# Kernel optimization log

Measured on AMD Instinct MI355X. Metric: run time of the kernel, lower is better.

## Reference

```python
import jax, jax.numpy as jnp
import numpy as np

N, DIN = 8192, 768
DH1, DO1 = 64, 64
DH2, DO2 = 32, 64


def setup_inputs() -> dict:
    key = jax.random.key(0)
    ks = jax.random.split(key, 12)
    s = lambda *sh: 0.02
    inp = {
        "X": jax.random.normal(ks[0], (N, DIN), jnp.float32),
        "A": jax.random.randint(ks[1], (N, N), 0, 2, jnp.int32),
        # GAT layer 1: W (din->dh), a (2dh), W2 (dh->dout) + bias
        "W1": jax.random.normal(ks[2], (DIN, DH1), jnp.float32) * 0.02,
        "a1": jax.random.normal(ks[3], (2 * DH1,), jnp.float32) * 0.02,
        "W21": jax.random.normal(ks[4], (DH1, DO1), jnp.float32) * 0.02,
        "b21": jnp.zeros((DO1,), jnp.float32),
        # GAT layer 2
        "Wg2": jax.random.normal(ks[5], (DO1, DH2), jnp.float32) * 0.02,
        "a2": jax.random.normal(ks[6], (2 * DH2,), jnp.float32) * 0.02,
        "W22": jax.random.normal(ks[7], (DH2, DO2), jnp.float32) * 0.02,
        "b22": jnp.zeros((DO2,), jnp.float32),
        # MLP head: 64 -> 64 -> 2
        "M1": jax.random.normal(ks[8], (DO2, 64), jnp.float32) * 0.02,
        "bm1": jnp.zeros((64,), jnp.float32),
        "M2": jax.random.normal(ks[9], (64, 2), jnp.float32) * 0.02,
        "bm2": jnp.zeros((2,), jnp.float32),
    }
    return inp


def _tiny_gat(X, A, W, a, W2, b2):
    # H = X @ W; e_ij = a . [H_i, H_j] = H_i@a_src + H_j@a_dst (same math,
    # no N x N x 2dh intermediate)
    H = X @ W                      # [N, dh]
    dh = W.shape[1]
    e = (H @ a[:dh])[:, None] + (H @ a[dh:])[None, :]   # [N, N]
    e = jnp.where(A == 0, jnp.float32(-1e9), e)
    alpha = jax.nn.softmax(e, axis=1)                   # softmax over neighbors j
    Z = alpha @ H                                       # [N, dh]
    return jax.nn.elu(Z @ W2 + b2)


def reference(X, A, W1, a1, W21, b21, Wg2, a2, W22, b22, M1, bm1, M2, bm2):
    Z = _tiny_gat(X, A, W1, a1, W21, b21)    # [N, 64]
    Z = _tiny_gat(Z, A, Wg2, a2, W22, b22)   # [N, 64]
    g = Z.mean(axis=0)                       # [64]
    h = jax.nn.relu(g @ M1 + bm1)
    return h @ M2 + bm2                      # [2]
```

## Files before the change

### kernel.cpp

```cpp
#include <hip/hip_runtime.h>


#define NN 8192

typedef __attribute__((ext_vector_type(8))) short s16x8;
typedef __attribute__((ext_vector_type(4))) float f32x4;
union V16 { uint4 u; s16x8 s; };

static constexpr size_t OFF_WBITS = 0;
static constexpr size_t OFF_GT1H  = (size_t)8 << 20;
static constexpr size_t OFF_GT1L  = ((size_t)9 << 20) + 512 * 1024;
static constexpr size_t OFF_GT2H  = (size_t)11 << 20;
static constexpr size_t OFF_GT2L  = (size_t)12 << 20;
static constexpr size_t OFF_GPART = (size_t)13 << 20;
static constexpr size_t OFF_NUMP  = (size_t)16 << 20;
static constexpr size_t OFF_DP    = (size_t)40 << 20;

__device__ __forceinline__ float elu_f(float x) {
    return x > 0.f ? x : expm1f(x);
}
__device__ __forceinline__ unsigned int bf16_rne(float x) {
    unsigned int u = __float_as_uint(x);
    return (u + 0x7FFFu + ((u >> 16) & 1u)) >> 16;
}
__device__ __forceinline__ unsigned int split_pack(float g) {
    unsigned int hi = bf16_rne(g);
    float fhi = __uint_as_float(hi << 16);
    unsigned int lo = bf16_rne(g - fhi);
    return (hi << 16) | lo;
}
__device__ __forceinline__ void split3(float f, unsigned int& h, unsigned int& m,
                                       unsigned int& l) {
    h = bf16_rne(f);
    float fh = __uint_as_float(h << 16);
    float r1 = f - fh;
    m = bf16_rne(r1);
    float fm = __uint_as_float(m << 16);
    l = bf16_rne(r1 - fm);
}
__device__ __forceinline__ unsigned int bits2bf(unsigned int b2) {
    return (b2 & 1u) * 0x3F80u + (b2 & 2u) * 0x1FC00000u;
}

__global__ __launch_bounds__(256) void k_xw1m(const float* __restrict__ X,
                                              const float* __restrict__ W1,
                                              float* __restrict__ Dp) {
    __shared__ unsigned int fh[6144];
    __shared__ unsigned int fl[6144];
    const int tid = threadIdx.x, wv = tid >> 6, lane = tid & 63;
    const int ks = blockIdx.y;
    for (int i = tid; i < 6144; i += 256) {
        const int feat = i & 63, kp = i >> 6;
        const int kg = ks * 192 + 2 * kp;
        float w0 = W1[(size_t)kg * 64 + feat];
        float w1 = W1[(size_t)(kg + 1) * 64 + feat];
        unsigned int h0 = bf16_rne(w0);
        unsigned int l0 = bf16_rne(w0 - __uint_as_float(h0 << 16));
        unsigned int h1 = bf16_rne(w1);
        unsigned int l1 = bf16_rne(w1 - __uint_as_float(h1 << 16));
        const int mt = feat >> 4, n = feat & 15;
        const int ktl = kp >> 4, rem = kp & 15, quad = rem >> 2, q = rem & 3;
        const int idx = ((mt * 6 + ktl) * 64 + quad * 16 + n) * 4 + q;
        fh[idx] = h0 | (h1 << 16);
        fl[idx] = l0 | (l1 << 16);
    }
    __syncthreads();
    const int n = lane & 15, quad = lane >> 4;
    const int node = blockIdx.x * 64 + wv * 16 + n;
    const int ntg = blockIdx.x * 4 + wv;
    f32x4 acc[4];
#pragma unroll
    for (int mt = 0; mt < 4; ++mt) acc[mt] = (f32x4){0.f, 0.f, 0.f, 0.f};
    const float4* X4 = (const float4*)X;
    for (int kk = 0; kk < 6; ++kk) {
        const int ktg = ks * 6 + kk;
        float4 x01 = X4[(size_t)node * 192 + ktg * 8 + quad * 2];
        float4 x23 = X4[(size_t)node * 192 + ktg * 8 + quad * 2 + 1];
        float xf[8] = {x01.x, x01.y, x01.z, x01.w, x23.x, x23.y, x23.z, x23.w};
        V16 bh, bm, bl;
        unsigned int* bhp = (unsigned int*)&bh.u;
        unsigned int* bmp = (unsigned int*)&bm.u;
        unsigned int* blp = (unsigned int*)&bl.u;
#pragma unroll
        for (int q = 0; q < 4; ++q) {
            unsigned int h0, m0, l0, h1, m1, l1;
            split3(xf[2 * q], h0, m0, l0);
            split3(xf[2 * q + 1], h1, m1, l1);
            bhp[q] = h0 | (h1 << 16);
            bmp[q] = m0 | (m1 << 16);
            blp[q] = l0 | (l1 << 16);
        }
#pragma unroll
        for (int mt = 0; mt < 4; ++mt) {
            const int base = ((mt * 6 + kk) * 64 + lane) * 4;
            V16 awh, awl;
            awh.u = *(const uint4*)&fh[base];
            awl.u = *(const uint4*)&fl[base];
            acc[mt] = __builtin_amdgcn_mfma_f32_16x16x32_bf16(awh.s, bh.s, acc[mt], 0, 0, 0);
            acc[mt] = __builtin_amdgcn_mfma_f32_16x16x32_bf16(awh.s, bm.s, acc[mt], 0, 0, 0);
            acc[mt] = __builtin_amdgcn_mfma_f32_16x16x32_bf16(awh.s, bl.s, acc[mt], 0, 0, 0);
            acc[mt] = __builtin_amdgcn_mfma_f32_16x16x32_bf16(awl.s, bh.s, acc[mt], 0, 0, 0);
            acc[mt] = __builtin_amdgcn_mfma_f32_16x16x32_bf16(awl.s, bm.s, acc[mt], 0, 0, 0);
        }
    }
#pragma unroll
    for (int mt = 0; mt < 4; ++mt)
        *(f32x4*)&Dp[(size_t)(((ks * 4 + mt) * 512 + ntg) * 64 + lane) * 4] = acc[mt];
}

__global__ __launch_bounds__(256) void k_xcomb(const float* __restrict__ Dp,
                                               const float* __restrict__ a1,
                                               unsigned int* __restrict__ Gt1h,
                                               unsigned int* __restrict__ Gt1l) {
    __shared__ float Hsh[64][33];
    __shared__ float us[32];
    const int tid = threadIdx.x;
    if (tid < 128) {
        const int ntl = tid >> 6, lane = tid & 63;
        const int n = lane & 15, quad = lane >> 4;
        const int ntg = blockIdx.x * 2 + ntl;
        float dpart = 0.f;
#pragma unroll
        for (int mt = 0; mt < 4; ++mt) {
            float v[4] = {0.f, 0.f, 0.f, 0.f};
#pragma unroll
            for (int ksp = 0; ksp < 4; ++ksp) {
                const float* p = &Dp[(size_t)(((ksp * 4 + mt) * 512 + ntg) * 64 + lane) * 4];
                v[0] += p[0]; v[1] += p[1]; v[2] += p[2]; v[3] += p[3];
            }
#pragma unroll
            for (int r = 0; r < 4; ++r) {
                int feat = mt * 16 + quad * 4 + r;
                Hsh[feat][ntl * 16 + n] = v[r];
                dpart += v[r] * a1[64 + feat];
            }
        }
        dpart += __shfl_xor(dpart, 16);
        dpart += __shfl_xor(dpart, 32);
        float uu = expf(dpart);
        if (lane < 16) us[ntl * 16 + lane] = uu;
    }
    __syncthreads();
    {
        const int mt = tid >> 6, lane = tid & 63;
        const int feat = mt * 16 + (lane & 15), quad = lane >> 4;
        uint4 hv, lv;
        unsigned int g0, g1;
#define PACK_Q(Q, FX)                                                   \
        {                                                               \
            int j0 = quad * 8 + 2 * Q;                                  \
            g0 = split_pack(us[j0] * Hsh[feat][j0]);                    \
            g1 = split_pack(us[j0 + 1] * Hsh[feat][j0 + 1]);            \
            hv.FX = (g0 >> 16) | (g1 & 0xFFFF0000u);                    \
            lv.FX = (g0 & 0xFFFFu) | (g1 << 16);                        \
        }
        PACK_Q(0, x) PACK_Q(1, y) PACK_Q(2, z) PACK_Q(3, w)
#undef PACK_Q
        size_t base = ((size_t)(mt * 256 + blockIdx.x) * 64 + lane) * 4;
        *(uint4*)(Gt1h + base) = hv;
        *(uint4*)(Gt1l + base) = lv;
    }
    if (tid < 64) {
        const int ml = tid & 15, quad = tid >> 4;
        uint4 hv, lv;
        unsigned int g0, g1;
#define PACK_Q(Q, FX)                                                   \
        {                                                               \
            int j0 = quad * 8 + 2 * Q;                                  \
            if (ml == 0) { g0 = split_pack(us[j0]);                     \
                           g1 = split_pack(us[j0 + 1]); }               \
            else { g0 = 0; g1 = 0; }                                    \
            hv.FX = (g0 >> 16) | (g1 & 0xFFFF0000u);                    \
            lv.FX = (g0 & 0xFFFFu) | (g1 << 16);                        \
        }
        PACK_Q(0, x) PACK_Q(1, y) PACK_Q(2, z) PACK_Q(3, w)
#undef PACK_Q
        size_t base = ((size_t)(4 * 256 + blockIdx.x) * 64 + tid) * 4;
        *(uint4*)(Gt1h + base) = hv;
        *(uint4*)(Gt1l + base) = lv;
    }
}

__global__ __launch_bounds__(320) void k_attn1f(const int* __restrict__ A,
                                                const unsigned int* __restrict__ Gt1h,
                                                const unsigned int* __restrict__ Gt1l,
                                                unsigned int* __restrict__ Wb32,
                                                float* __restrict__ num1p) {
    __shared__ unsigned int bw[64 * 33];
    const int tid = threadIdx.x, wv = tid >> 6, lane = tid & 63;
    const int node0 = blockIdx.x * 64;
    const int kc = blockIdx.y;
    if (wv < 4) {
        unsigned short* msh = (unsigned short*)bw;
        for (int rr = 0; rr < 16; ++rr) {
            const int r = wv * 16 + rr;
            const int4* A4 = (const int4*)(A + (size_t)(node0 + r) * NN + kc * 1024 + lane * 16);
            int4 a0 = A4[0], a1 = A4[1], a2 = A4[2], a3 = A4[3];
            unsigned int m0 = 0;
            m0 |= ((a0.x != 0) << 0)  | ((a0.y != 0) << 1)  |
                  ((a0.z != 0) << 2)  | ((a0.w != 0) << 3);
            m0 |= ((a1.x != 0) << 4)  | ((a1.y != 0) << 5)  |
                  ((a1.z != 0) << 6)  | ((a1.w != 0) << 7);
            m0 |= ((a2.x != 0) << 8)  | ((a2.y != 0) << 9)  |
                  ((a2.z != 0) << 10) | ((a2.w != 0) << 11);
            m0 |= ((a3.x != 0) << 12) | ((a3.y != 0) << 13) |
                  ((a3.z != 0) << 14) | ((a3.w != 0) << 15);
            msh[r * 66 + lane] = (unsigned short)m0;
        }
    }
    __syncthreads();
    if (tid < 256) {
        const int r = tid >> 2, part = tid & 3;
        uint4 v0, v1;
        v0.x = bw[r * 33 + part * 8 + 0]; v0.y = bw[r * 33 + part * 8 + 1];
        v0.z = bw[r * 33 + part * 8 + 2]; v0.w = bw[r * 33 + part * 8 + 3];
        v1.x = bw[r * 33 + part * 8 + 4]; v1.y = bw[r * 33 + part * 8 + 5];
        v1.z = bw[r * 33 + part * 8 + 6]; v1.w = bw[r * 33 + part * 8 + 7];
        uint4* dst = (uint4*)(Wb32 + (size_t)(node0 + r) * 256 + kc * 32 + part * 8);
        dst[0] = v0; dst[1] = v1;
    }
    const int n = lane & 15, quad = lane >> 4;
    const int mt = wv;
    const int kt0 = kc * 32;
    f32x4 acc[4];
#pragma unroll
    for (int nt = 0; nt < 4; ++nt) acc[nt] = (f32x4){0.f, 0.f, 0.f, 0.f};
#pragma unroll 4
    for (int ks = 0; ks < 32; ++ks) {
        size_t base = ((size_t)(mt * 256 + kt0 + ks) * 64 + lane) * 4;
        V16 ah, al;
        ah.u = *(const uint4*)(Gt1h + base);
        al.u = *(const uint4*)(Gt1l + base);
#pragma unroll
        for (int nt = 0; nt < 4; ++nt) {
            unsigned int by8 = (bw[(nt * 16 + n) * 33 + ks] >> (quad * 8)) & 0xFFu;
            V16 bf;
            bf.u = make_uint4(bits2bf(by8), bits2bf(by8 >> 2),
                              bits2bf(by8 >> 4), bits2bf(by8 >> 6));
            acc[nt] = __builtin_amdgcn_mfma_f32_16x16x32_bf16(ah.s, bf.s, acc[nt], 0, 0, 0);
            acc[nt] = __builtin_amdgcn_mfma_f32_16x16x32_bf16(al.s, bf.s, acc[nt], 0, 0, 0);
        }
    }
    const int s = blockIdx.y;
#pragma unroll
    for (int nt = 0; nt < 4; ++nt) {
        const int node = node0 + nt * 16 + n;
        *(f32x4*)&num1p[((size_t)s * NN + node) * 80 + mt * 16 + quad * 4] = acc[nt];
    }
}

__global__ __launch_bounds__(256) void k_ep1(const float* __restrict__ num1p,
                                             const float* __restrict__ W21,
                                             const float* __restrict__ b21,
                                             const float* __restrict__ Wg2,
                                             const float* __restrict__ a2,
                                             unsigned int* __restrict__ Gt2h,
                                             unsigned int* __restrict__ Gt2l) {
    __shared__ float w21sh[64 * 64];
    __shared__ float wg2sh[64 * 32];
    __shared__ float zsh[4][64];
    __shared__ float osh[4][64];
    __shared__ unsigned int g2sh[32][9];
    __shared__ unsigned int u2sh[8];
    const int tid = threadIdx.x, wv = tid >> 6, lane = tid & 63;
    const int node0 = blockIdx.x * 8;
    {
        const float4* s4 = (const float4*)W21;
        float4* d4 = (float4*)w21sh;
        d4[tid] = s4[tid];
        d4[tid + 256] = s4[tid + 256];
        d4[tid + 512] = s4[tid + 512];
        d4[tid + 768] = s4[tid + 768];
        ((float4*)wg2sh)[tid] = ((const float4*)Wg2)[tid];
        ((float4*)wg2sh)[tid + 256] = ((const float4*)Wg2)[tid + 256];
    }
    const float bb = b21[lane];
    const int l32 = lane & 31;
    const float a2v = (lane < 32) ? a2[32 + l32] : 0.f;
    __syncthreads();
    for (int it = 0; it < 2; ++it) {
        const int node = node0 + wv * 2 + it;
        float sacc = 0.f, dnum = 0.f;
#pragma unroll
        for (int sp = 0; sp < 8; ++sp) {
            const float* base = &num1p[((size_t)sp * NN + node) * 80];
            sacc += base[lane];
            dnum += base[64];
        }
        zsh[wv][lane] = sacc / dnum;
        __builtin_amdgcn_wave_barrier();
        const float4* zv = (const float4*)&zsh[wv][0];
        float o0 = 0.f, o1 = 0.f;
#pragma unroll 4
        for (int c4 = 0; c4 < 16; ++c4) {
            float4 z4 = zv[c4];
            const int c = c4 * 4;
            o0 += z4.x * w21sh[(c + 0) * 64 + lane] + z4.y * w21sh[(c + 1) * 64 + lane];
            o1 += z4.z * w21sh[(c + 2) * 64 + lane] + z4.w * w21sh[(c + 3) * 64 + lane];
        }
        float o = elu_f(bb + o0 + o1);
        osh[wv][lane] = o;
        __builtin_amdgcn_wave_barrier();
        const float4* ov = (const float4*)&osh[wv][0];
        float h0 = 0.f, h1 = 0.f;
#pragma unroll 4
        for (int c4 = 0; c4 < 16; ++c4) {
            float4 o4 = ov[c4];
            const int c = c4 * 4;
            h0 += o4.x * wg2sh[(c + 0) * 32 + l32] + o4.y * wg2sh[(c + 1) * 32 + l32];
            h1 += o4.z * wg2sh[(c + 2) * 32 + l32] + o4.w * wg2sh[(c + 3) * 32 + l32];
        }
        float hval = h0 + h1;
        float pp = hval * a2v;
#pragma unroll
        for (int off = 32; off; off >>= 1) pp += __shfl_down(pp, off);
        float d2 = __shfl(pp, 0);
        float uu = expf(d2);
        const int nodeloc = wv * 2 + it;
        if (lane == 0) u2sh[nodeloc] = split_pack(uu);
        if (lane < 32) g2sh[l32][nodeloc] = split_pack(uu * hval);
    }
    __syncthreads();
    if (tid < 48) {
        const int mt = tid >> 4, ml = tid & 15;
        const int quad_w = blockIdx.x & 3, kt = blockIdx.x >> 2;
        const int lane2 = quad_w * 16 + ml;
        uint4 hv, lv;
        unsigned int g0, g1;
#define PACK_Q(Q, F)                                                   \
        {                                                              \
            int j0 = 2 * Q;                                            \
            if (mt < 2) { g0 = g2sh[mt * 16 + ml][j0];                 \
                          g1 = g2sh[mt * 16 + ml][j0 + 1]; }           \
            else if (ml == 0) { g0 = u2sh[j0]; g1 = u2sh[j0 + 1]; }    \
            else { g0 = 0; g1 = 0; }                                   \
            hv.F = (g0 >> 16) | (g1 & 0xFFFF0000u);                    \
            lv.F = (g0 & 0xFFFFu) | (g1 << 16);                        \
        }
        PACK_Q(0, x) PACK_Q(1, y) PACK_Q(2, z) PACK_Q(3, w)
#undef PACK_Q
        size_t base = ((size_t)(mt * 256 + kt) * 64 + lane2) * 4;
        *(uint4*)(Gt2h + base) = hv;
        *(uint4*)(Gt2l + base) = lv;
    }
}

__global__ __launch_bounds__(256) void k_attn2(const unsigned int* __restrict__ Wb32,
                                               const unsigned int* __restrict__ Gt2h,
                                               const unsigned int* __restrict__ Gt2l,
                                               float* __restrict__ num2p) {
    __shared__ unsigned int bw[64 * 36];
    const int tid = threadIdx.x, wv = tid >> 6, lane = tid & 63;
    const int node0 = blockIdx.x * 64;
    const int kt0 = blockIdx.y * 32;
    {
        const int r = tid >> 2, part = tid & 3;
        const uint4* src = (const uint4*)(Wb32 + (size_t)(node0 + r) * 256 + kt0 + part * 8);
        uint4 v0 = src[0], v1 = src[1];
        *(uint4*)&bw[r * 36 + part * 8] = v0;
        *(uint4*)&bw[r * 36 + part * 8 + 4] = v1;
    }
    __syncthreads();
    if (wv == 3) return;
    const int n = lane & 15, quad = lane >> 4;
    const int mt = wv;
    f32x4 acc[4];
#pragma unroll
    for (int nt = 0; nt < 4; ++nt) acc[nt] = (f32x4){0.f, 0.f, 0.f, 0.f};
#pragma unroll 4
    for (int ks = 0; ks < 32; ++ks) {
        size_t base = ((size_t)(mt * 256 + kt0 + ks) * 64 + lane) * 4;
        V16 ah, al;
        ah.u = *(const uint4*)(Gt2h + base);
        al.u = *(const uint4*)(Gt2l + base);
#pragma unroll
        for (int nt = 0; nt < 4; ++nt) {
            unsigned int by8 = (bw[(nt * 16 + n) * 36 + ks] >> (quad * 8)) & 0xFFu;
            V16 bf;
            bf.u = make_uint4(bits2bf(by8), bits2bf(by8 >> 2),
                              bits2bf(by8 >> 4), bits2bf(by8 >> 6));
            acc[nt] = __builtin_amdgcn_mfma_f32_16x16x32_bf16(ah.s, bf.s, acc[nt], 0, 0, 0);
            acc[nt] = __builtin_amdgcn_mfma_f32_16x16x32_bf16(al.s, bf.s, acc[nt], 0, 0, 0);
        }
    }
    const int s = blockIdx.y;
#pragma unroll
    for (int nt = 0; nt < 4; ++nt) {
        const int node = node0 + nt * 16 + n;
        *(f32x4*)&num2p[((size_t)s * NN + node) * 48 + mt * 16 + quad * 4] = acc[nt];
    }
}

__global__ __launch_bounds__(512) void k_ep2(const float* __restrict__ num2p,
                                             const float* __restrict__ W22,
                                             const float* __restrict__ b22,
                                             float* __restrict__ gpart) {
    __shared__ float w22sh[32 * 64];
    __shared__ float zsh[8][32];
    __shared__ float gsh[8][64];
    const int tid = threadIdx.x, wv = tid >> 6, lane = tid & 63;
    ((float4*)w22sh)[tid] = ((const float4*)W22)[tid];
    const float bb = b22[lane];
    __syncthreads();
    float greg = 0.f;
    for (int it = 0; it < 4; ++it) {
        const int row = blockIdx.x * 32 + wv * 4 + it;
        float val = 0.f;
        if (lane < 33) {
#pragma unroll
            for (int sp = 0; sp < 8; ++sp)
                val += num2p[((size_t)sp * NN + row) * 48 + lane];
        }
        float den = __shfl(val, 32);
        if (lane < 32) zsh[wv][lane] = val / den;
        __builtin_amdgcn_wave_barrier();
        const float4* zv = (const float4*)&zsh[wv][0];
        float o0 = 0.f, o1 = 0.f;
#pragma unroll 4
        for (int c4 = 0; c4 < 8; ++c4) {
            float4 z4 = zv[c4];
            const int c = c4 * 4;
            o0 += z4.x * w22sh[(c + 0) * 64 + lane] + z4.y * w22sh[(c + 1) * 64 + lane];
            o1 += z4.z * w22sh[(c + 2) * 64 + lane] + z4.w * w22sh[(c + 3) * 64 + lane];
        }
        greg += elu_f(bb + o0 + o1);
        __builtin_amdgcn_wave_barrier();
    }
    gsh[wv][lane] = greg;
    __syncthreads();
    if (tid < 64) {
        float s = 0.f;
#pragma unroll
        for (int w = 0; w < 8; ++w) s += gsh[w][tid];
        gpart[(size_t)blockIdx.x * 64 + tid] = s;
    }
}

__global__ __launch_bounds__(256) void k_head(const float* __restrict__ gpart,
                                              const float* __restrict__ M1,
                                              const float* __restrict__ bm1,
                                              const float* __restrict__ M2,
                                              const float* __restrict__ bm2,
                                              float* __restrict__ outp) {
    __shared__ float part[4][64];
    __shared__ float gsh[64];
    __shared__ float hsh[64];
    const int tid = threadIdx.x, col = tid & 63, p = tid >> 6;
    float s = 0.f;
    for (int b = p * 64; b < p * 64 + 64; ++b)
        s += gpart[(size_t)b * 64 + col];
    part[p][col] = s;
    __syncthreads();
    if (tid < 64)
        gsh[tid] = (part[0][tid] + part[1][tid] + part[2][tid] + part[3][tid])
                   * (1.0f / 8192.0f);
    __syncthreads();
    if (tid < 64) {
        float h = bm1[tid];
        for (int c = 0; c < 64; ++c) h += gsh[c] * M1[c * 64 + tid];
        hsh[tid] = h > 0.f ? h : 0.f;
    }
    __syncthreads();
    if (tid < 2) {
        float o = bm2[tid];
        for (int j = 0; j < 64; ++j) o += hsh[j] * M2[j * 2 + tid];
        outp[tid] = o;
    }
}

extern "C" void kernel_launch(void* const* d_in, const int* in_sizes, int n_in,
                              void* d_out, int out_size, void* d_ws, size_t ws_size,
                              hipStream_t stream) {
    const float* X   = (const float*)d_in[0];
    const int*   A   = (const int*)  d_in[1];
    const float* W1  = (const float*)d_in[2];
    const float* a1  = (const float*)d_in[3];
    const float* W21 = (const float*)d_in[4];
    const float* b21 = (const float*)d_in[5];
    const float* Wg2 = (const float*)d_in[6];
    const float* a2  = (const float*)d_in[7];
    const float* W22 = (const float*)d_in[8];
    const float* b22 = (const float*)d_in[9];
    const float* M1  = (const float*)d_in[10];
    const float* bm1 = (const float*)d_in[11];
    const float* M2  = (const float*)d_in[12];
    const float* bm2 = (const float*)d_in[13];
    float* out = (float*)d_out;

    char* ws = (char*)d_ws;
    unsigned int* Wbits = (unsigned int*)(ws + OFF_WBITS);
    unsigned int* Gt1h  = (unsigned int*)(ws + OFF_GT1H);
    unsigned int* Gt1l  = (unsigned int*)(ws + OFF_GT1L);
    unsigned int* Gt2h  = (unsigned int*)(ws + OFF_GT2H);
    unsigned int* Gt2l  = (unsigned int*)(ws + OFF_GT2L);
    float* Dp    = (float*)(ws + OFF_DP);
    float* gpart = (float*)(ws + OFF_GPART);
    float* nump  = (float*)(ws + OFF_NUMP);

    k_xw1m  <<<dim3(128, 4), 256, 0, stream>>>(X, W1, Dp);
    k_xcomb <<<256, 256, 0, stream>>>(Dp, a1, Gt1h, Gt1l);
    k_attn1f<<<dim3(128, 8), 320, 0, stream>>>(A, Gt1h, Gt1l, Wbits, nump);
    k_ep1   <<<1024, 256, 0, stream>>>(nump, W21, b21, Wg2, a2, Gt2h, Gt2l);
    k_attn2 <<<dim3(128, 8), 256, 0, stream>>>(Wbits, Gt2h, Gt2l, nump);
    k_ep2   <<<256, 512, 0, stream>>>(nump, W22, b22, gpart);
    k_head  <<<1, 256, 0, stream>>>(gpart, M1, bm1, M2, bm2, out);
}
```

Measured before the change: 507.3 us.

## Move adjacency bit-packing into front kernel alongside X@W1 projection

Adjacency-to-bitmask packing moves out of the layer-1 attention kernel and into a combined front kernel. Its 2048 extra blocks each pack four rows of A and run concurrently with the X@W1 split-bf16 MFMA blocks. The attention kernel now loads precomputed bitmasks from global memory into padded shared memory and goes straight to its MFMA loop. The goal is to overlap the 256MB int32 adjacency read with the projection work. The cost is an extra bitmask round-trip through global memory and a larger, heterogeneous front grid.

```diff
diff --git a/kernel.cpp b/kernel.cpp
--- a/kernel.cpp
+++ b/kernel.cpp
@@ -42,13 +42,44 @@
     return (b2 & 1u) * 0x3F80u + (b2 & 2u) * 0x1FC00000u;
 }
 
-__global__ __launch_bounds__(256) void k_xw1m(const float* __restrict__ X,
-                                              const float* __restrict__ W1,
-                                              float* __restrict__ Dp) {
-    __shared__ unsigned int fh[6144];
-    __shared__ unsigned int fl[6144];
+__global__ __launch_bounds__(256) void k_front(const float* __restrict__ X,
+                                               const float* __restrict__ W1,
+                                               const int* __restrict__ A,
+                                               float* __restrict__ Dp,
+                                               unsigned int* __restrict__ Wb32) {
+    __shared__ unsigned int smem[12288];
     const int tid = threadIdx.x, wv = tid >> 6, lane = tid & 63;
-    const int ks = blockIdx.y;
+    if (blockIdx.x >= 512) {
+        unsigned short* msh = (unsigned short*)smem;
+        const int pb = blockIdx.x - 512;
+        const int row0 = pb * 4;
+        const int row = row0 + wv;
+        for (int c = 0; c < 8; ++c) {
+            const int j = c * 1024 + lane * 16;
+            const int4* A4 = (const int4*)(A + (size_t)row * NN + j);
+            int4 a0 = A4[0], a1 = A4[1], a2 = A4[2], a3 = A4[3];
+            unsigned int m0 = 0;
+            m0 |= ((a0.x != 0) << 0)  | ((a0.y != 0) << 1)  |
+                  ((a0.z != 0) << 2)  | ((a0.w != 0) << 3);
+            m0 |= ((a1.x != 0) << 4)  | ((a1.y != 0) << 5)  |
+                  ((a1.z != 0) << 6)  | ((a1.w != 0) << 7);
+            m0 |= ((a2.x != 0) << 8)  | ((a2.y != 0) << 9)  |
+                  ((a2.z != 0) << 10) | ((a2.w != 0) << 11);
+            m0 |= ((a3.x != 0) << 12) | ((a3.y != 0) << 13) |
+                  ((a3.z != 0) << 14) | ((a3.w != 0) << 15);
+            msh[wv * 512 + c * 64 + lane] = (unsigned short)m0;
+        }
+        __syncthreads();
+        const int r = tid >> 6, i = tid & 63;
+        const uint4* src = (const uint4*)&msh[r * 512];
+        uint4* dst = (uint4*)(Wb32 + (size_t)(row0 + r) * 256);
+        dst[i] = src[i];
+        return;
+    }
+    unsigned int* fh = smem;
+    unsigned int* fl = smem + 6144;
+    const int ng = blockIdx.x & 127;
+    const int ks = blockIdx.x >> 7;
     for (int i = tid; i < 6144; i += 256) {
         const int feat = i & 63, kp = i >> 6;
         const int kg = ks * 192 + 2 * kp;
@@ -66,8 +97,8 @@
     }
     __syncthreads();
     const int n = lane & 15, quad = lane >> 4;
-    const int node = blockIdx.x * 64 + wv * 16 + n;
-    const int ntg = blockIdx.x * 4 + wv;
+    const int node = ng * 64 + wv * 16 + n;
+    const int ntg = ng * 4 + wv;
     f32x4 acc[4];
 #pragma unroll
     for (int mt = 0; mt < 4; ++mt) acc[mt] = (f32x4){0.f, 0.f, 0.f, 0.f};
@@ -181,47 +212,24 @@
     }
 }
 
-__global__ __launch_bounds__(320) void k_attn1f(const int* __restrict__ A,
-                                                const unsigned int* __restrict__ Gt1h,
-                                                const unsigned int* __restrict__ Gt1l,
-                                                unsigned int* __restrict__ Wb32,
-                                                float* __restrict__ num1p) {
-    __shared__ unsigned int bw[64 * 33];
+__global__ __launch_bounds__(320) void k_attn1(const unsigned int* __restrict__ Wb32,
+                                               const unsigned int* __restrict__ Gt1h,
+                                               const unsigned int* __restrict__ Gt1l,
+                                               float* __restrict__ num1p) {
+    __shared__ unsigned int bw[64 * 36];
     const int tid = threadIdx.x, wv = tid >> 6, lane = tid & 63;
     const int node0 = blockIdx.x * 64;
-    const int kc = blockIdx.y;
-    if (wv < 4) {
-        unsigned short* msh = (unsigned short*)bw;
-        for (int rr = 0; rr < 16; ++rr) {
-            const int r = wv * 16 + rr;
-            const int4* A4 = (const int4*)(A + (size_t)(node0 + r) * NN + kc * 1024 + lane * 16);
-            int4 a0 = A4[0], a1 = A4[1], a2 = A4[2], a3 = A4[3];
-            unsigned int m0 = 0;
-            m0 |= ((a0.x != 0) << 0)  | ((a0.y != 0) << 1)  |
-                  ((a0.z != 0) << 2)  | ((a0.w != 0) << 3);
-            m0 |= ((a1.x != 0) << 4)  | ((a1.y != 0) << 5)  |
-                  ((a1.z != 0) << 6)  | ((a1.w != 0) << 7);
-            m0 |= ((a2.x != 0) << 8)  | ((a2.y != 0) << 9)  |
-                  ((a2.z != 0) << 10) | ((a2.w != 0) << 11);
-            m0 |= ((a3.x != 0) << 12) | ((a3.y != 0) << 13) |
-                  ((a3.z != 0) << 14) | ((a3.w != 0) << 15);
-            msh[r * 66 + lane] = (unsigned short)m0;
-        }
-    }
-    __syncthreads();
+    const int kt0 = blockIdx.y * 32;
     if (tid < 256) {
         const int r = tid >> 2, part = tid & 3;
-        uint4 v0, v1;
-        v0.x = bw[r * 33 + part * 8 + 0]; v0.y = bw[r * 33 + part * 8 + 1];
-        v0.z = bw[r * 33 + part * 8 + 2]; v0.w = bw[r * 33 + part * 8 + 3];
-        v1.x = bw[r * 33 + part * 8 + 4]; v1.y = bw[r * 33 + part * 8 + 5];
-        v1.z = bw[r * 33 + part * 8 + 6]; v1.w = bw[r * 33 + part * 8 + 7];
-        uint4* dst = (uint4*)(Wb32 + (size_t)(node0 + r) * 256 + kc * 32 + part * 8);
-        dst[0] = v0; dst[1] = v1;
-    }
+        const uint4* src = (const uint4*)(Wb32 + (size_t)(node0 + r) * 256 + kt0 + part * 8);
+        uint4 v0 = src[0], v1 = src[1];
+        *(uint4*)&bw[r * 36 + part * 8] = v0;
+        *(uint4*)&bw[r * 36 + part * 8 + 4] = v1;
+    }
+    __syncthreads();
     const int n = lane & 15, quad = lane >> 4;
     const int mt = wv;
-    const int kt0 = kc * 32;
     f32x4 acc[4];
 #pragma unroll
     for (int nt = 0; nt < 4; ++nt) acc[nt] = (f32x4){0.f, 0.f, 0.f, 0.f};
@@ -233,7 +241,7 @@
         al.u = *(const uint4*)(Gt1l + base);
 #pragma unroll
         for (int nt = 0; nt < 4; ++nt) {
-            unsigned int by8 = (bw[(nt * 16 + n) * 33 + ks] >> (quad * 8)) & 0xFFu;
+            unsigned int by8 = (bw[(nt * 16 + n) * 36 + ks] >> (quad * 8)) & 0xFFu;
             V16 bf;
             bf.u = make_uint4(bits2bf(by8), bits2bf(by8 >> 2),
                               bits2bf(by8 >> 4), bits2bf(by8 >> 6));
@@ -497,9 +505,9 @@
     float* gpart = (float*)(ws + OFF_GPART);
     float* nump  = (float*)(ws + OFF_NUMP);
 
-    k_xw1m  <<<dim3(128, 4), 256, 0, stream>>>(X, W1, Dp);
+    k_front <<<2560, 256, 0, stream>>>(X, W1, A, Dp, Wbits);
     k_xcomb <<<256, 256, 0, stream>>>(Dp, a1, Gt1h, Gt1l);
-    k_attn1f<<<dim3(128, 8), 320, 0, stream>>>(A, Gt1h, Gt1l, Wbits, nump);
+    k_attn1 <<<dim3(128, 8), 320, 0, stream>>>(Wbits, Gt1h, Gt1l, nump);
     k_ep1   <<<1024, 256, 0, stream>>>(nump, W21, b21, Wg2, a2, Gt2h, Gt2l);
     k_attn2 <<<dim3(128, 8), 256, 0, stream>>>(Wbits, Gt2h, Gt2l, nump);
     k_ep2   <<<256, 512, 0, stream>>>(nump, W22, b22, gpart);
```

New measurement: 513.2 us. About the same (+1.2%).
